# Optimization experiments

Measured on AMD Instinct MI355X. Metric: run time of the kernel, lower is better.

The kernel has to match this reference:

```python
import jax, jax.numpy as jnp
import numpy as np

B, C, H, W = 8, 128, 128, 128
HEADS = 8

def setup_inputs() -> dict:
    key = jax.random.key(0)
    k1, k2 = jax.random.split(key)
    x1 = jax.random.normal(k1, (B, C, H, W), dtype=jnp.float32)
    x2 = jax.random.normal(k2, (B, C, H, W), dtype=jnp.float32)
    return {"x1": x1, "x2": x2}

def reference(x1, x2):
    b, c, h, w = x1.shape
    n = h * w
    hk = c // HEADS  # head key channels
    hv = c // HEADS  # head value channels
    # [B,C,N] layouts (channels-first, as in torch after transpose back)
    vals = x1.reshape(b, c, n)   # values come from x1
    kq = x2.reshape(b, c, n)     # keys and queries come from x2
    k = kq.reshape(b, HEADS, hk, n)
    v = vals.reshape(b, HEADS, hv, n)
    key_sm = jax.nn.softmax(k, axis=-1)   # softmax over N (torch dim=2)
    query_sm = jax.nn.softmax(k, axis=2)  # softmax over head channels (torch dim=1)
    # context = key @ value^T : [B,h,hk,hv]
    context = jnp.einsum('bhkn,bhvn->bhkv', key_sm, v)
    # attended = context^T @ query : [B,h,hv,N]
    attended = jnp.einsum('bhkv,bhkn->bhvn', context, query_sm)
    return attended.reshape(b, c, H, W)
```

## Files before the change

kernel.cpp:

```cpp
#include <hip/hip_runtime.h>
#include <math.h>

#define N_     16384
#define N4     4096
#define BHN    64
#define CH     16
#define CHUNKS 16

#define WS_PART 0
#define WS_ZP   (BHN * CHUNKS * 256)

typedef __attribute__((ext_vector_type(8))) short short8;
typedef __attribute__((ext_vector_type(4))) float f32x4;

static __device__ __forceinline__ short f2bf(float f) {
    __bf16 b = (__bf16)f;
    return __builtin_bit_cast(short, b);
}

static __device__ __forceinline__ void gload16(const float* g, float* l) {
    __builtin_amdgcn_global_load_lds(
        (const __attribute__((address_space(1))) unsigned int*)g,
        (__attribute__((address_space(3))) unsigned int*)l, 16, 0, 0);
}

__global__ __launch_bounds__(256, 4) void k_ctx_mfma(const float* __restrict__ x1,
                                                     const float* __restrict__ x2,
                                                     float* __restrict__ ws) {
    int chunk = blockIdx.x;
    int bh    = blockIdx.y;
    int tid   = threadIdx.x;
    int w = tid >> 6, l = tid & 63;

    __shared__ float ka_s[2][16 * 128];
    __shared__ float va_s[2][16 * 128];
    __shared__ float cred[4][256];
    __shared__ float zred[4][16];

    int half = l >> 5;
    int u    = l & 31;
    int rowA = 4 * w + half;
    int rowB = 4 * w + 2 + half;
    int vA = u ^ ((rowA & 7) << 1);
    int vB = u ^ ((rowB & 7) << 1);
    const float* gk0 = x2 + (size_t)(bh * CH + rowA) * N_ + chunk * 1024 + vA * 4;
    const float* gk1 = x2 + (size_t)(bh * CH + rowB) * N_ + chunk * 1024 + vB * 4;
    const float* gv0 = x1 + (size_t)(bh * CH + rowA) * N_ + chunk * 1024 + vA * 4;
    const float* gv1 = x1 + (size_t)(bh * CH + rowB) * N_ + chunk * 1024 + vB * 4;

    int row  = l & 15;
    int v0   = w * 8 + (l >> 4) * 2;
    int u0   = v0 ^ ((row & 7) << 1);
    int offr = row * 128 + u0 * 4;

    f32x4 acc = {0.f, 0.f, 0.f, 0.f};
    float zacc = 0.f;

#define STAGE(b, t) do {                                         \
        gload16(gk0 + (t) * 128, &ka_s[b][(2 * w)     * 256]);   \
        gload16(gk1 + (t) * 128, &ka_s[b][(2 * w + 1) * 256]);   \
        gload16(gv0 + (t) * 128, &va_s[b][(2 * w)     * 256]);   \
        gload16(gv1 + (t) * 128, &va_s[b][(2 * w + 1) * 256]);   \
    } while (0)

    STAGE(0, 0);
    asm volatile("s_waitcnt vmcnt(0)" ::: "memory");
    __syncthreads();

    for (int t = 0; t < 8; ++t) {
        int b = t & 1;
        if (t < 7) STAGE(1 - b, t + 1);

        float4 kq0 = *(const float4*)&ka_s[b][offr];
        float4 kq1 = *(const float4*)&ka_s[b][offr + 4];
        float4 vq0 = *(const float4*)&va_s[b][offr];
        float4 vq1 = *(const float4*)&va_s[b][offr + 4];
        float e0 = __expf(kq0.x), e1 = __expf(kq0.y), e2 = __expf(kq0.z), e3 = __expf(kq0.w);
        float e4 = __expf(kq1.x), e5 = __expf(kq1.y), e6 = __expf(kq1.z), e7 = __expf(kq1.w);
        zacc += ((e0 + e1) + (e2 + e3)) + ((e4 + e5) + (e6 + e7));
        short8 af = {f2bf(e0), f2bf(e1), f2bf(e2), f2bf(e3),
                     f2bf(e4), f2bf(e5), f2bf(e6), f2bf(e7)};
        short8 bv = {f2bf(vq0.x), f2bf(vq0.y), f2bf(vq0.z), f2bf(vq0.w),
                     f2bf(vq1.x), f2bf(vq1.y), f2bf(vq1.z), f2bf(vq1.w)};
        acc = __builtin_amdgcn_mfma_f32_16x16x32_bf16(af, bv, acc, 0, 0, 0);

        if (t < 7) {
            asm volatile("s_waitcnt vmcnt(0)" ::: "memory");
            __syncthreads();
        }
    }
#undef STAGE

    zacc += __shfl_xor(zacc, 16);
    zacc += __shfl_xor(zacc, 32);
    if (l < 16) zred[w][l] = zacc;

    #pragma unroll
    for (int r = 0; r < 4; ++r)
        cred[w][((l >> 4) * 4 + r) * 16 + row] = acc[r];
    __syncthreads();

    if (tid < 16) {
        float zz = (zred[0][tid] + zred[1][tid]) + (zred[2][tid] + zred[3][tid]);
        ws[WS_ZP + (bh * CHUNKS + chunk) * 16 + tid] = zz;
    }
    float c = (cred[0][tid] + cred[1][tid]) + (cred[2][tid] + cred[3][tid]);
    ws[WS_PART + (size_t)(bh * CHUNKS + chunk) * 256 + tid] = c;
}

__global__ __launch_bounds__(256) void k_attend(const float* __restrict__ x2,
                                                const float* __restrict__ ws,
                                                float* __restrict__ out) {
    int cb  = blockIdx.x;
    int bh  = blockIdx.y;
    int tid = threadIdx.x;

    __shared__ float q_s[16][256];
    __shared__ float ctxs[256];
    __shared__ float rzs[16];

    float csum = 0.f;
    #pragma unroll
    for (int c = 0; c < CHUNKS; ++c)
        csum += ws[WS_PART + (size_t)(bh * CHUNKS + c) * 256 + tid];
    if (tid < 16) {
        float z = 0.f;
        #pragma unroll
        for (int c = 0; c < CHUNKS; ++c)
            z += ws[WS_ZP + (bh * CHUNKS + c) * 16 + tid];
        rzs[tid] = 1.0f / z;
    }

    const float4* px = (const float4*)(x2 + (size_t)bh * CH * N_);
    int base4 = cb * 64;
    #pragma unroll
    for (int r = 0; r < 4; ++r) {
        int idx = r * 256 + tid;
        int ch = idx >> 6, j = idx & 63;
        float4 v = px[(size_t)ch * N4 + base4 + j];
        *(float4*)&q_s[ch][j * 4] = v;
    }
    __syncthreads();

    ctxs[tid] = csum * rzs[tid >> 4];

    {
        int col = tid;
        float kv[16];
        #pragma unroll
        for (int c = 0; c < 16; ++c) kv[c] = q_s[c][col];
        float mx = kv[0];
        #pragma unroll
        for (int c = 1; c < 16; ++c) mx = fmaxf(mx, kv[c]);
        float s = 0.f;
        #pragma unroll
        for (int c = 0; c < 16; ++c) { kv[c] = __expf(kv[c] - mx); s += kv[c]; }
        float rs = 1.0f / s;
        #pragma unroll
        for (int c = 0; c < 16; ++c) q_s[c][col] = kv[c] * rs;
    }
    __syncthreads();

    int vg = tid >> 6, cq = tid & 63;
    int vv0 = vg * 4, c0 = cq * 4;
    float4 a0 = make_float4(0.f,0.f,0.f,0.f);
    float4 a1 = a0, a2 = a0, a3 = a0;
    #pragma unroll
    for (int kk = 0; kk < 16; ++kk) {
        float4 cx = *(const float4*)&ctxs[kk * 16 + vv0];
        float4 q4 = *(const float4*)&q_s[kk][c0];
        a0.x = fmaf(q4.x, cx.x, a0.x); a0.y = fmaf(q4.x, cx.y, a0.y);
        a0.z = fmaf(q4.x, cx.z, a0.z); a0.w = fmaf(q4.x, cx.w, a0.w);
        a1.x = fmaf(q4.y, cx.x, a1.x); a1.y = fmaf(q4.y, cx.y, a1.y);
        a1.z = fmaf(q4.y, cx.z, a1.z); a1.w = fmaf(q4.y, cx.w, a1.w);
        a2.x = fmaf(q4.z, cx.x, a2.x); a2.y = fmaf(q4.z, cx.y, a2.y);
        a2.z = fmaf(q4.z, cx.z, a2.z); a2.w = fmaf(q4.z, cx.w, a2.w);
        a3.x = fmaf(q4.w, cx.x, a3.x); a3.y = fmaf(q4.w, cx.y, a3.y);
        a3.z = fmaf(q4.w, cx.z, a3.z); a3.w = fmaf(q4.w, cx.w, a3.w);
    }
    size_t outbase = (size_t)bh * CH * N_ + (size_t)cb * 256 + c0;
    float4 o;
    o = make_float4(a0.x, a1.x, a2.x, a3.x);
    *(float4*)&out[outbase + (size_t)(vv0 + 0) * N_] = o;
    o = make_float4(a0.y, a1.y, a2.y, a3.y);
    *(float4*)&out[outbase + (size_t)(vv0 + 1) * N_] = o;
    o = make_float4(a0.z, a1.z, a2.z, a3.z);
    *(float4*)&out[outbase + (size_t)(vv0 + 2) * N_] = o;
    o = make_float4(a0.w, a1.w, a2.w, a3.w);
    *(float4*)&out[outbase + (size_t)(vv0 + 3) * N_] = o;
}

extern "C" void kernel_launch(void* const* d_in, const int* in_sizes, int n_in,
                              void* d_out, int out_size, void* d_ws, size_t ws_size,
                              hipStream_t stream) {
    const float* x1 = (const float*)d_in[0];
    const float* x2 = (const float*)d_in[1];
    float* out = (float*)d_out;
    float* ws  = (float*)d_ws;

    k_ctx_mfma <<<dim3(CHUNKS, BHN), 256, 0, stream>>>(x1, x2, ws);
    k_attend   <<<dim3(64, BHN),     256, 0, stream>>>(x2, ws, out);
}
```

Baseline: 51.40 us.

## Issue all chunk loads upfront and drain with staged vmcnt waits

The context kernel now uses twice as many chunks of half the length. Each block issues all four sub-tile global-to-LDS loads at once into four LDS buffers, then processes them in order with decreasing vmcnt waits and barriers. This replaces the double-buffered loop that waited for all outstanding loads on every step. The swizzle changes from a shifted XOR to a plain XOR on float4 units. The aim is to keep more loads in flight and put more blocks on the grid, at the cost of doubled LDS per block, a lower occupancy hint, and twice as many partial results for k_attend to reduce.

```diff
diff --git a/kernel.cpp b/kernel.cpp
--- a/kernel.cpp
+++ b/kernel.cpp
@@ -5,7 +5,7 @@
 #define N4     4096
 #define BHN    64
 #define CH     16
-#define CHUNKS 16
+#define CHUNKS 32
 
 #define WS_PART 0
 #define WS_ZP   (BHN * CHUNKS * 256)
@@ -24,7 +24,7 @@
         (__attribute__((address_space(3))) unsigned int*)l, 16, 0, 0);
 }
 
-__global__ __launch_bounds__(256, 4) void k_ctx_mfma(const float* __restrict__ x1,
+__global__ __launch_bounds__(256, 2) void k_ctx_mfma(const float* __restrict__ x1,
                                                      const float* __restrict__ x2,
                                                      float* __restrict__ ws) {
     int chunk = blockIdx.x;
@@ -32,8 +32,8 @@
     int tid   = threadIdx.x;
     int w = tid >> 6, l = tid & 63;
 
-    __shared__ float ka_s[2][16 * 128];
-    __shared__ float va_s[2][16 * 128];
+    __shared__ float ka_s[4][2048];
+    __shared__ float va_s[4][2048];
     __shared__ float cred[4][256];
     __shared__ float zred[4][16];
 
@@ -41,55 +41,56 @@
     int u    = l & 31;
     int rowA = 4 * w + half;
     int rowB = 4 * w + 2 + half;
-    int vA = u ^ ((rowA & 7) << 1);
-    int vB = u ^ ((rowB & 7) << 1);
-    const float* gk0 = x2 + (size_t)(bh * CH + rowA) * N_ + chunk * 1024 + vA * 4;
-    const float* gk1 = x2 + (size_t)(bh * CH + rowB) * N_ + chunk * 1024 + vB * 4;
-    const float* gv0 = x1 + (size_t)(bh * CH + rowA) * N_ + chunk * 1024 + vA * 4;
-    const float* gv1 = x1 + (size_t)(bh * CH + rowB) * N_ + chunk * 1024 + vB * 4;
-
-    int row  = l & 15;
-    int v0   = w * 8 + (l >> 4) * 2;
-    int u0   = v0 ^ ((row & 7) << 1);
-    int offr = row * 128 + u0 * 4;
+    int vA = u ^ (rowA & 7);
+    int vB = u ^ (rowB & 7);
+    const float* gk0 = x2 + (size_t)(bh * CH + rowA) * N_ + chunk * 512 + vA * 4;
+    const float* gk1 = x2 + (size_t)(bh * CH + rowB) * N_ + chunk * 512 + vB * 4;
+    const float* gv0 = x1 + (size_t)(bh * CH + rowA) * N_ + chunk * 512 + vA * 4;
+    const float* gv1 = x1 + (size_t)(bh * CH + rowB) * N_ + chunk * 512 + vB * 4;
+
+    #pragma unroll
+    for (int t = 0; t < 4; ++t) {
+        gload16(gk0 + t * 128, &ka_s[t][(2 * w)     * 256]);
+        gload16(gk1 + t * 128, &ka_s[t][(2 * w + 1) * 256]);
+        gload16(gv0 + t * 128, &va_s[t][(2 * w)     * 256]);
+        gload16(gv1 + t * 128, &va_s[t][(2 * w + 1) * 256]);
+    }
+
+    int row = l & 15;
+    int key = row & 7;
+    int v0  = w * 8 + (l >> 4) * 2;
+    int off0 = (row * 32 + ((v0    ) ^ key)) * 4;
+    int off1 = (row * 32 + ((v0 + 1) ^ key)) * 4;
 
     f32x4 acc = {0.f, 0.f, 0.f, 0.f};
     float zacc = 0.f;
 
-#define STAGE(b, t) do {                                         \
-        gload16(gk0 + (t) * 128, &ka_s[b][(2 * w)     * 256]);   \
-        gload16(gk1 + (t) * 128, &ka_s[b][(2 * w + 1) * 256]);   \
-        gload16(gv0 + (t) * 128, &va_s[b][(2 * w)     * 256]);   \
-        gload16(gv1 + (t) * 128, &va_s[b][(2 * w + 1) * 256]);   \
-    } while (0)
-
-    STAGE(0, 0);
-    asm volatile("s_waitcnt vmcnt(0)" ::: "memory");
-    __syncthreads();
-
-    for (int t = 0; t < 8; ++t) {
-        int b = t & 1;
-        if (t < 7) STAGE(1 - b, t + 1);
-
-        float4 kq0 = *(const float4*)&ka_s[b][offr];
-        float4 kq1 = *(const float4*)&ka_s[b][offr + 4];
-        float4 vq0 = *(const float4*)&va_s[b][offr];
-        float4 vq1 = *(const float4*)&va_s[b][offr + 4];
-        float e0 = __expf(kq0.x), e1 = __expf(kq0.y), e2 = __expf(kq0.z), e3 = __expf(kq0.w);
-        float e4 = __expf(kq1.x), e5 = __expf(kq1.y), e6 = __expf(kq1.z), e7 = __expf(kq1.w);
-        zacc += ((e0 + e1) + (e2 + e3)) + ((e4 + e5) + (e6 + e7));
-        short8 af = {f2bf(e0), f2bf(e1), f2bf(e2), f2bf(e3),
-                     f2bf(e4), f2bf(e5), f2bf(e6), f2bf(e7)};
-        short8 bv = {f2bf(vq0.x), f2bf(vq0.y), f2bf(vq0.z), f2bf(vq0.w),
-                     f2bf(vq1.x), f2bf(vq1.y), f2bf(vq1.z), f2bf(vq1.w)};
-        acc = __builtin_amdgcn_mfma_f32_16x16x32_bf16(af, bv, acc, 0, 0, 0);
-
-        if (t < 7) {
-            asm volatile("s_waitcnt vmcnt(0)" ::: "memory");
-            __syncthreads();
-        }
-    }
-#undef STAGE
+#define PHASE(T, VMS)                                                          \
+    {                                                                          \
+        asm volatile("s_waitcnt vmcnt(" VMS ")" ::: "memory");                 \
+        __builtin_amdgcn_s_barrier();                                          \
+        __builtin_amdgcn_sched_barrier(0);                                     \
+        float4 kq0 = *(const float4*)&ka_s[T][off0];                           \
+        float4 kq1 = *(const float4*)&ka_s[T][off1];                           \
+        float4 vq0 = *(const float4*)&va_s[T][off0];                           \
+        float4 vq1 = *(const float4*)&va_s[T][off1];                           \
+        float e0 = __expf(kq0.x), e1 = __expf(kq0.y),                          \
+              e2 = __expf(kq0.z), e3 = __expf(kq0.w);                          \
+        float e4 = __expf(kq1.x), e5 = __expf(kq1.y),                          \
+              e6 = __expf(kq1.z), e7 = __expf(kq1.w);                          \
+        zacc += ((e0 + e1) + (e2 + e3)) + ((e4 + e5) + (e6 + e7));             \
+        short8 af = {f2bf(e0), f2bf(e1), f2bf(e2), f2bf(e3),                   \
+                     f2bf(e4), f2bf(e5), f2bf(e6), f2bf(e7)};                  \
+        short8 bv = {f2bf(vq0.x), f2bf(vq0.y), f2bf(vq0.z), f2bf(vq0.w),       \
+                     f2bf(vq1.x), f2bf(vq1.y), f2bf(vq1.z), f2bf(vq1.w)};      \
+        acc = __builtin_amdgcn_mfma_f32_16x16x32_bf16(af, bv, acc, 0, 0, 0);   \
+    }
+
+    PHASE(0, "12")
+    PHASE(1, "8")
+    PHASE(2, "4")
+    PHASE(3, "0")
+#undef PHASE
 
     zacc += __shfl_xor(zacc, 16);
     zacc += __shfl_xor(zacc, 32);
```

Result: slower. 53.66 us (+4.4%).
